# Optimization experiments

Hardware: AMD Instinct MI355X
Metric: run time of the kernel (lower is better)

The kernel has to match this reference:

```python
import jax, jax.numpy as jnp
import numpy as np

N, H, W, C, K = 8, 512, 512, 3, 5
PAD = K // 2  # odd square kernel, 'same' zero padding


def setup_inputs() -> dict:
    key = jax.random.key(0)
    k1, k2 = jax.random.split(key)
    input_data = jax.random.normal(k1, (N, H, W, C), dtype=jnp.float32)
    # per-sample, per-pixel unshared kernels: (N, H, W, K*K)
    weights = jax.random.normal(k2, (N, H, W, K * K), dtype=jnp.float32) * 0.1
    return {"input_data": input_data, "weights": weights}


def reference(input_data, weights):
    # Local (untied) depthwise conv: out[n,h,w,c] =
    #   sum_{dh,dw} in[n, h+dh-P, w+dw-P, c] * weights[n, h, w, dh*K+dw]
    # Weight is shared across channels (no channel dim in weights).
    x = jnp.pad(input_data, ((0, 0), (PAD, PAD), (PAD, PAD), (0, 0)))
    out = jnp.zeros_like(input_data)
    for k in range(K * K):  # fixed small loop over kernel taps
        dh, dw = k // K, k % K
        out = out + x[:, dh:dh + H, dw:dw + W, :] * weights[..., k:k + 1]
    return out
```

## Files before the change

kernel.cpp:

```cpp
#include <hip/hip_runtime.h>

#define NN 8
#define HH 512
#define WW 512
#define CC 3
#define KK 5
#define PADP 2
#define WROWF (WW * CC)
#define NBLOCKS (NN * HH * WW / 128)

typedef float f4a __attribute__((ext_vector_type(4), aligned(4)));

struct Row { f4a L0, L1, L2, L3; };

__device__ __forceinline__ void load_row(const float* rb, Row& r) {
    r.L0 = *(const f4a*)(rb);
    r.L1 = *(const f4a*)(rb + 4);
    r.L2 = *(const f4a*)(rb + 8);
    r.L3 = *(const f4a*)(rb + 11);
}

__device__ __forceinline__ void fma_row(const Row& r, const float* wp,
                                        float& a0, float& a1, float& a2) {
    const float w0 = wp[0], w1 = wp[1], w2 = wp[2], w3 = wp[3], w4 = wp[4];
    a0 = fmaf(r.L0[0], w0, a0); a1 = fmaf(r.L0[1], w0, a1); a2 = fmaf(r.L0[2], w0, a2);
    a0 = fmaf(r.L0[3], w1, a0); a1 = fmaf(r.L1[0], w1, a1); a2 = fmaf(r.L1[1], w1, a2);
    a0 = fmaf(r.L1[2], w2, a0); a1 = fmaf(r.L1[3], w2, a1); a2 = fmaf(r.L2[0], w2, a2);
    a0 = fmaf(r.L2[1], w3, a0); a1 = fmaf(r.L2[2], w3, a1); a2 = fmaf(r.L2[3], w3, a2);
    a0 = fmaf(r.L3[1], w4, a0); a1 = fmaf(r.L3[2], w4, a1); a2 = fmaf(r.L3[3], w4, a2);
}

#define GLDS16(gp, lp) __builtin_amdgcn_global_load_lds( \
    (const __attribute__((address_space(1))) void*)(gp), \
    (__attribute__((address_space(3))) void*)(lp), 16, 0, 0)
#define GLDS4(gp, lp) __builtin_amdgcn_global_load_lds( \
    (const __attribute__((address_space(1))) void*)(gp), \
    (__attribute__((address_space(3))) void*)(lp), 4, 0, 0)

__global__ __launch_bounds__(64, 3) void conv_local_kernel(
    const float* __restrict__ in,
    const float* __restrict__ wt,
    float* __restrict__ out)
{
    __shared__ float w_lds[2 * 64 * KK * KK];

    const int lane = threadIdx.x;
    const int b    = ((blockIdx.x & 7) << 11) | (blockIdx.x >> 3);
    const int wseg = b & 7;
    const int hp   = (b >> 3) & 255;
    const int n    = b >> 11;
    const int w0   = wseg << 6;
    const int h0   = hp << 1;

    const long pix0 = ((long)(n * HH + h0)) * WW + w0;
    const long pix1 = pix0 + WW;
    const float* inb = in + (size_t)n * (HH * WW * CC);

    {
        const char* s0 = (const char*)(wt + pix0 * (KK * KK));
        const char* s1 = (const char*)(wt + pix1 * (KK * KK));
#pragma unroll
        for (int it = 0; it < 6; ++it)
            GLDS16(s0 + it * 1024 + lane * 16, &w_lds[it * 256]);
        GLDS4(s0 + 6144 + lane * 4, &w_lds[1536]);
#pragma unroll
        for (int it = 0; it < 6; ++it)
            GLDS16(s1 + it * 1024 + lane * 16, &w_lds[1600 + it * 256]);
        GLDS4(s1 + 6144 + lane * 4, &w_lds[1600 + 1536]);
    }

    const float* wp0 = &w_lds[lane * (KK * KK)];
    const float* wp1 = &w_lds[1600 + lane * (KK * KK)];

    const bool fast = (w0 != 0) && (w0 != WW - 64) && (h0 >= PADP) && (h0 <= HH - 4);

    if (fast) {
        const float* rb = inb + ((long)(h0 - PADP) * WW + (w0 + lane - PADP)) * CC;
        Row A, B;
        load_row(rb, A);
        load_row(rb + WROWF, B);
        asm volatile("s_waitcnt vmcnt(0)" ::: "memory");

        float a0 = 0.f, a1 = 0.f, a2 = 0.f;
        float c0 = 0.f, c1 = 0.f, c2 = 0.f;

        fma_row(A, wp0 + 0, a0, a1, a2);
        load_row(rb + 2 * WROWF, A);
        fma_row(B, wp0 + 5, a0, a1, a2);
        fma_row(B, wp1 + 0, c0, c1, c2);
        load_row(rb + 3 * WROWF, B);
        fma_row(A, wp0 + 10, a0, a1, a2);
        fma_row(A, wp1 + 5, c0, c1, c2);
        load_row(rb + 4 * WROWF, A);
        fma_row(B, wp0 + 15, a0, a1, a2);
        fma_row(B, wp1 + 10, c0, c1, c2);
        load_row(rb + 5 * WROWF, B);
        fma_row(A, wp0 + 20, a0, a1, a2);
        fma_row(A, wp1 + 15, c0, c1, c2);
        fma_row(B, wp1 + 20, c0, c1, c2);

        float* o0 = out + (pix0 + lane) * CC;
        o0[0] = a0; o0[1] = a1; o0[2] = a2;
        float* o1 = out + (pix1 + lane) * CC;
        o1[0] = c0; o1[1] = c1; o1[2] = c2;
    } else {
        asm volatile("s_waitcnt vmcnt(0)" ::: "memory");
#pragma unroll
        for (int px = 0; px < 2; ++px) {
            const int hh = h0 + px;
            const int w  = w0 + lane;
            const float* wp = px ? wp1 : wp0;
            float a0 = 0.f, a1 = 0.f, a2 = 0.f;
#pragma unroll
            for (int dh = 0; dh < KK; ++dh) {
                const int ih = hh + dh - PADP;
                const bool rok = ((unsigned)ih < (unsigned)HH);
#pragma unroll
                for (int dw = 0; dw < KK; ++dw) {
                    const int iw = w + dw - PADP;
                    const bool ok = rok && ((unsigned)iw < (unsigned)WW);
                    const float* p = inb + ((long)(ih * WW + iw)) * CC;
                    float v0 = ok ? p[0] : 0.f;
                    float v1 = ok ? p[1] : 0.f;
                    float v2 = ok ? p[2] : 0.f;
                    const float wv = wp[dh * KK + dw];
                    a0 = fmaf(v0, wv, a0);
                    a1 = fmaf(v1, wv, a1);
                    a2 = fmaf(v2, wv, a2);
                }
            }
            float* o = out + (((long)(n * HH + hh)) * WW + w) * CC;
            o[0] = a0; o[1] = a1; o[2] = a2;
        }
    }
}

extern "C" void kernel_launch(void* const* d_in, const int* in_sizes, int n_in,
                              void* d_out, int out_size, void* d_ws, size_t ws_size,
                              hipStream_t stream) {
    const float* in = (const float*)d_in[0];
    const float* wt = (const float*)d_in[1];
    float* out = (float*)d_out;

    conv_local_kernel<<<NBLOCKS, 64, 0, stream>>>(in, wt, out);
}
```

Measured before the change: 58.95 us.

## Compute one output row per wave with two waves per block

Each 64-lane wave now handles a single output row instead of two adjacent rows, and two waves share a 128-thread block with separate LDS weight buffers. The aim is more waves in flight and a shorter per-thread dependency chain, giving better latency hiding and occupancy. The cost is that the vertical input-row reuse between the two rows is lost: each output row now loads 5 input rows instead of 6 loads serving 2 rows. Scheduling barriers are also added after the wait on the loads.

```diff
diff --git a/kernel.cpp b/kernel.cpp
--- a/kernel.cpp
+++ b/kernel.cpp
@@ -7,7 +7,7 @@
 #define KK 5
 #define PADP 2
 #define WROWF (WW * CC)
-#define NBLOCKS (NN * HH * WW / 128)
+#define NBLOCKS 16384
 
 typedef float f4a __attribute__((ext_vector_type(4), aligned(4)));
 
@@ -37,101 +37,81 @@
     (const __attribute__((address_space(1))) void*)(gp), \
     (__attribute__((address_space(3))) void*)(lp), 4, 0, 0)
 
-__global__ __launch_bounds__(64, 3) void conv_local_kernel(
+__global__ __launch_bounds__(128, 6) void conv_local_kernel(
     const float* __restrict__ in,
     const float* __restrict__ wt,
     float* __restrict__ out)
 {
-    __shared__ float w_lds[2 * 64 * KK * KK];
+    __shared__ float w_lds[2][64 * KK * KK];
 
-    const int lane = threadIdx.x;
-    const int b    = ((blockIdx.x & 7) << 11) | (blockIdx.x >> 3);
-    const int wseg = b & 7;
-    const int hp   = (b >> 3) & 255;
-    const int n    = b >> 11;
-    const int w0   = wseg << 6;
-    const int h0   = hp << 1;
+    const int lane = threadIdx.x & 63;
+    const int wv   = threadIdx.x >> 6;
+    const int bs = ((blockIdx.x & 7) << 11) | (blockIdx.x >> 3);
+    const int t  = (bs << 1) | wv;
+    const int w0 = (t & 7) << 6;
+    const int h  = (t >> 3) & (HH - 1);
+    const int n  = t >> 12;
 
-    const long pix0 = ((long)(n * HH + h0)) * WW + w0;
-    const long pix1 = pix0 + WW;
+    const long pix0 = ((long)(n * HH + h)) * WW + w0;
     const float* inb = in + (size_t)n * (HH * WW * CC);
 
     {
         const char* s0 = (const char*)(wt + pix0 * (KK * KK));
-        const char* s1 = (const char*)(wt + pix1 * (KK * KK));
+        float* wl = w_lds[wv];
 #pragma unroll
         for (int it = 0; it < 6; ++it)
-            GLDS16(s0 + it * 1024 + lane * 16, &w_lds[it * 256]);
-        GLDS4(s0 + 6144 + lane * 4, &w_lds[1536]);
-#pragma unroll
-        for (int it = 0; it < 6; ++it)
-            GLDS16(s1 + it * 1024 + lane * 16, &w_lds[1600 + it * 256]);
-        GLDS4(s1 + 6144 + lane * 4, &w_lds[1600 + 1536]);
+            GLDS16(s0 + it * 1024 + lane * 16, wl + it * 256);
+        GLDS4(s0 + 6144 + lane * 4, wl + 1536);
     }
 
-    const float* wp0 = &w_lds[lane * (KK * KK)];
-    const float* wp1 = &w_lds[1600 + lane * (KK * KK)];
-
-    const bool fast = (w0 != 0) && (w0 != WW - 64) && (h0 >= PADP) && (h0 <= HH - 4);
+    const float* wp = &w_lds[wv][lane * (KK * KK)];
+    const bool fast = (w0 != 0) && (w0 != WW - 64) && (h >= PADP) && (h < HH - PADP);
 
     if (fast) {
-        const float* rb = inb + ((long)(h0 - PADP) * WW + (w0 + lane - PADP)) * CC;
+        const float* rb = inb + ((long)(h - PADP) * WW + (w0 + lane - PADP)) * CC;
         Row A, B;
         load_row(rb, A);
-        load_row(rb + WROWF, B);
+        load_row(rb + 1 * WROWF, B);
         asm volatile("s_waitcnt vmcnt(0)" ::: "memory");
+        __builtin_amdgcn_sched_barrier(0);
 
         float a0 = 0.f, a1 = 0.f, a2 = 0.f;
-        float c0 = 0.f, c1 = 0.f, c2 = 0.f;
+        fma_row(A, wp + 0,  a0, a1, a2);
+        load_row(rb + 2 * WROWF, A);
+        fma_row(B, wp + 5,  a0, a1, a2);
+        load_row(rb + 3 * WROWF, B);
+        fma_row(A, wp + 10, a0, a1, a2);
+        load_row(rb + 4 * WROWF, A);
+        fma_row(B, wp + 15, a0, a1, a2);
+        fma_row(A, wp + 20, a0, a1, a2);
 
-        fma_row(A, wp0 + 0, a0, a1, a2);
-        load_row(rb + 2 * WROWF, A);
-        fma_row(B, wp0 + 5, a0, a1, a2);
-        fma_row(B, wp1 + 0, c0, c1, c2);
-        load_row(rb + 3 * WROWF, B);
-        fma_row(A, wp0 + 10, a0, a1, a2);
-        fma_row(A, wp1 + 5, c0, c1, c2);
-        load_row(rb + 4 * WROWF, A);
-        fma_row(B, wp0 + 15, a0, a1, a2);
-        fma_row(B, wp1 + 10, c0, c1, c2);
-        load_row(rb + 5 * WROWF, B);
-        fma_row(A, wp0 + 20, a0, a1, a2);
-        fma_row(A, wp1 + 15, c0, c1, c2);
-        fma_row(B, wp1 + 20, c0, c1, c2);
-
-        float* o0 = out + (pix0 + lane) * CC;
-        o0[0] = a0; o0[1] = a1; o0[2] = a2;
-        float* o1 = out + (pix1 + lane) * CC;
-        o1[0] = c0; o1[1] = c1; o1[2] = c2;
+        float* o = out + (pix0 + lane) * CC;
+        o[0] = a0; o[1] = a1; o[2] = a2;
     } else {
         asm volatile("s_waitcnt vmcnt(0)" ::: "memory");
+        __builtin_amdgcn_sched_barrier(0);
+        const int w = w0 + lane;
+        float a0 = 0.f, a1 = 0.f, a2 = 0.f;
 #pragma unroll
-        for (int px = 0; px < 2; ++px) {
-            const int hh = h0 + px;
-            const int w  = w0 + lane;
-            const float* wp = px ? wp1 : wp0;
-            float a0 = 0.f, a1 = 0.f, a2 = 0.f;
+        for (int dh = 0; dh < KK; ++dh) {
+            const int ih = h + dh - PADP;
+            const bool rok = ((unsigned)ih < (unsigned)HH);
 #pragma unroll
-            for (int dh = 0; dh < KK; ++dh) {
-                const int ih = hh + dh - PADP;
-                const bool rok = ((unsigned)ih < (unsigned)HH);
-#pragma unroll
-                for (int dw = 0; dw < KK; ++dw) {
-                    const int iw = w + dw - PADP;
-                    const bool ok = rok && ((unsigned)iw < (unsigned)WW);
-                    const float* p = inb + ((long)(ih * WW + iw)) * CC;
-                    float v0 = ok ? p[0] : 0.f;
-                    float v1 = ok ? p[1] : 0.f;
-                    float v2 = ok ? p[2] : 0.f;
-                    const float wv = wp[dh * KK + dw];
-                    a0 = fmaf(v0, wv, a0);
-                    a1 = fmaf(v1, wv, a1);
-                    a2 = fmaf(v2, wv, a2);
-                }
+            for (int dw = 0; dw < KK; ++dw) {
+                const int iw = w + dw - PADP;
+                const bool ok = rok && ((unsigned)iw < (unsigned)WW);
+                const float* p = inb + ((long)(ih * WW + iw)) * CC;
+                float v0 = ok ? p[0] : 0.f;
+                float v1 = ok ? p[1] : 0.f;
+                float v2 = ok ? p[2] : 0.f;
+                const float wv_ = wp[dh * KK + dw];
+                a0 = fmaf(v0, wv_, a0);
+                a1 = fmaf(v1, wv_, a1);
+                a2 = fmaf(v2, wv_, a2);
             }
-            float* o = out + (((long)(n * HH + hh)) * WW + w) * CC;
-            o[0] = a0; o[1] = a1; o[2] = a2;
         }
+        float* o = out + (pix0 + lane) * CC;
+        o[0] = a0; o[1] = a1; o[2] = a2;
     }
 }
 
@@ -142,5 +122,5 @@
     const float* wt = (const float*)d_in[1];
     float* out = (float*)d_out;
 
-    conv_local_kernel<<<NBLOCKS, 64, 0, stream>>>(in, wt, out);
+    conv_local_kernel<<<NBLOCKS, 128, 0, stream>>>(in, wt, out);
 }
```

Measured after the change: 124.7 us. +111.6%, slower.
